# Kernel tuning notes

Measured on AMD Instinct MI355X. Metric: run time of the kernel, lower is better.

The kernel has to match this reference:

```python
import jax, jax.numpy as jnp
import numpy as np

D = 2048
N_EXPERTS = 64
K = 2


def setup_inputs() -> dict:
    key = jax.random.key(0)
    kx, kw = jax.random.split(key)
    x = jax.random.normal(kx, (4, 4096, D), dtype=jnp.float32)
    # xavier_uniform for Linear(d, n_experts): bound = sqrt(6/(fan_in+fan_out))
    bound = float(np.sqrt(6.0 / (D + N_EXPERTS)))
    W = jax.random.uniform(kw, (N_EXPERTS, D), dtype=jnp.float32, minval=-bound, maxval=bound)
    b = jnp.zeros((N_EXPERTS,), dtype=jnp.float32)
    return {"x": x, "W": W, "b": b}


def reference(x, W, b):
    # logits: [B, S, E]  (eval mode: no noise)
    logits = jnp.einsum("bsd,ed->bse", x, W) + b
    topk_vals, topk_idx = jax.lax.top_k(logits, K)  # [B, S, K]
    gates = jax.nn.softmax(topk_vals, axis=-1)
    return gates, topk_idx
```

## Files before the change

kernel.cpp:

```cpp
#include <hip/hip_runtime.h>
#include <math.h>

#define DD 2048
#define EE 64
#define TM 32
#define BK 64
#define NCHUNK (DD / BK)
#define THREADS 512

#define ROWB 272
#define XPLANE (TM * ROWB)
#define WPLANE (EE * ROWB)
#define BUFB   (XPLANE + WPLANE)

typedef _Float16 f16x8 __attribute__((ext_vector_type(8)));
typedef float    f32x4 __attribute__((ext_vector_type(4)));

__device__ static inline void split8(const float4 a, const float4 b,
                                     f16x8& hi, f16x8& lo) {
    const float S = 32.f;
    const float v[8] = {a.x * S, a.y * S, a.z * S, a.w * S,
                        b.x * S, b.y * S, b.z * S, b.w * S};
#pragma unroll
    for (int i = 0; i < 8; ++i) {
        const _Float16 h = (_Float16)v[i];
        hi[i] = h;
        lo[i] = (_Float16)(v[i] - (float)h);
    }
}

__global__ __launch_bounds__(THREADS, 4) void router_kernel(
    const float* __restrict__ x, const float* __restrict__ W,
    const float* __restrict__ bias_g, float* __restrict__ out, int n_tokens)
{
    __shared__ __attribute__((aligned(16))) char  lds[2 * BUFB];
    __shared__ __attribute__((aligned(16))) float logits[TM * (EE + 1)];

    const int tid   = threadIdx.x;
    const int tBase = blockIdx.x * TM;

    const int sr = tid >> 3;
    const int sg = tid & 7;
    const bool do_x = (sr < TM);

    const float* xrow = x + (size_t)(tBase + (sr & (TM - 1))) * DD + sg * 8;
    const float* wrow = W + (size_t)sr * DD + sg * 8;

    float4 rx0 = {0,0,0,0}, rx1 = {0,0,0,0}, rw0, rw1;

#define LOADX(c) { if (do_x) { \
        rx0 = *(const float4*)&xrow[(c) * BK];     \
        rx1 = *(const float4*)&xrow[(c) * BK + 4]; } }
#define LOADW(c) { \
        rw0 = *(const float4*)&wrow[(c) * BK];     \
        rw1 = *(const float4*)&wrow[(c) * BK + 4]; }

#define WRITE_STAGE(buf) { \
    char* base = lds + (size_t)(buf) * BUFB; \
    { f16x8 hi, lo; split8(rw0, rw1, hi, lo); \
      const int off = XPLANE + sr * ROWB + sg * 32; \
      *(f16x8*)(base + off)      = hi; \
      *(f16x8*)(base + off + 16) = lo; } \
    if (do_x) { f16x8 hi, lo; split8(rx0, rx1, hi, lo); \
      const int off = sr * ROWB + sg * 32; \
      *(f16x8*)(base + off)      = hi; \
      *(f16x8*)(base + off + 16) = lo; } }

    const int wv   = tid >> 6;
    const int lane = tid & 63;
    const int mt   = wv & 1;
    const int nt   = wv >> 1;
    const int r16  = lane & 15;
    const int kg   = lane >> 4;

    const int aoff = (mt * 16 + r16) * ROWB + kg * 32;
    const int boff = XPLANE + (nt * 16 + r16) * ROWB + kg * 32;

    f32x4 acc = {0.f, 0.f, 0.f, 0.f};

#define COMPUTE(buf) { \
    const char* base = lds + (size_t)(buf) * BUFB; \
    _Pragma("unroll") for (int ks = 0; ks < 2; ++ks) { \
        const f16x8 ah = *(const f16x8*)(base + aoff + ks * 128); \
        const f16x8 al = *(const f16x8*)(base + aoff + ks * 128 + 16); \
        const f16x8 bh = *(const f16x8*)(base + boff + ks * 128); \
        const f16x8 bl = *(const f16x8*)(base + boff + ks * 128 + 16); \
        acc = __builtin_amdgcn_mfma_f32_16x16x32_f16(ah, bh, acc, 0, 0, 0); \
        acc = __builtin_amdgcn_mfma_f32_16x16x32_f16(al, bh, acc, 0, 0, 0); \
        acc = __builtin_amdgcn_mfma_f32_16x16x32_f16(ah, bl, acc, 0, 0, 0); \
    } }

    LOADX(0); LOADW(0);
    WRITE_STAGE(0);
    LOADX(1); LOADW(1);

    int cur = 0;
    for (int c = 0; c < NCHUNK; ++c) {
        __syncthreads();
        COMPUTE(cur);
        if (c + 1 < NCHUNK) {
            WRITE_STAGE(cur ^ 1);
            if (c + 2 < NCHUNK) { LOADX(c + 2); LOADW(c + 2); }
        }
        cur ^= 1;
    }

    __syncthreads();
    const int col  = nt * 16 + r16;
    const float bcol = bias_g[col];
    const float INV  = 1.f / 1024.f;
    const int rbase  = mt * 16 + kg * 4;
#pragma unroll
    for (int r = 0; r < 4; ++r)
        logits[(rbase + r) * (EE + 1) + col] = acc[r] * INV + bcol;
    __syncthreads();

    if (tid < TM) {
        const float* lrow = &logits[tid * (EE + 1)];
        float v1 = -INFINITY, v2 = -INFINITY;
        int   i1 = 0, i2 = 0;
        for (int e = 0; e < EE; ++e) {
            const float v = lrow[e];
            if (v > v1) { v2 = v1; i2 = i1; v1 = v; i1 = e; }
            else if (v > v2) { v2 = v; i2 = e; }
        }
        const float ed  = expf(v2 - v1);
        const float inv = 1.f / (1.f + ed);
        const int tok = tBase + tid;
        out[tok * 2 + 0] = inv;
        out[tok * 2 + 1] = ed * inv;
        float* oidx = out + (size_t)2 * n_tokens;
        oidx[tok * 2 + 0] = (float)i1;
        oidx[tok * 2 + 1] = (float)i2;
    }
}

extern "C" void kernel_launch(void* const* d_in, const int* in_sizes, int n_in,
                              void* d_out, int out_size, void* d_ws, size_t ws_size,
                              hipStream_t stream) {
    const float* x = (const float*)d_in[0];
    const float* W = (const float*)d_in[1];
    const float* b = (const float*)d_in[2];
    float* out = (float*)d_out;

    const int n_tokens = in_sizes[0] / DD;
    const int n_blocks = n_tokens / TM;

    router_kernel<<<n_blocks, THREADS, 0, stream>>>(x, W, b, out, n_tokens);
}
```

Before: 202.3 us.

## Double-buffer global prefetch registers and use lightweight LDS-only barriers

Splits the prefetch registers into two sets so global loads for chunk c+2 are issued before the compute of chunk c, deepening the load pipeline to two chunks in flight. The main loop is unrolled by two with fixed LDS buffer indices. __syncthreads is replaced by a barrier that waits only on LDS counters plus a scheduling barrier, so outstanding global loads need not drain at each sync. Costs extra VGPRs, which could hurt occupancy under the launch bound of 4.

Result: no change. 202.8 us (+0.2%).

```diff
diff --git a/kernel.cpp b/kernel.cpp
--- a/kernel.cpp
+++ b/kernel.cpp
@@ -15,6 +15,10 @@
 
 typedef _Float16 f16x8 __attribute__((ext_vector_type(8)));
 typedef float    f32x4 __attribute__((ext_vector_type(4)));
+
+#define BARRIER() { asm volatile("s_waitcnt lgkmcnt(0)" ::: "memory"); \
+                    __builtin_amdgcn_s_barrier(); \
+                    __builtin_amdgcn_sched_barrier(0); }
 
 __device__ static inline void split8(const float4 a, const float4 b,
                                      f16x8& hi, f16x8& lo) {
@@ -46,16 +50,17 @@
     const float* xrow = x + (size_t)(tBase + (sr & (TM - 1))) * DD + sg * 8;
     const float* wrow = W + (size_t)sr * DD + sg * 8;
 
-    float4 rx0 = {0,0,0,0}, rx1 = {0,0,0,0}, rw0, rw1;
+    float4 rxA0 = {0,0,0,0}, rxA1 = {0,0,0,0}, rwA0, rwA1;
+    float4 rxB0 = {0,0,0,0}, rxB1 = {0,0,0,0}, rwB0, rwB1;
 
-#define LOADX(c) { if (do_x) { \
-        rx0 = *(const float4*)&xrow[(c) * BK];     \
-        rx1 = *(const float4*)&xrow[(c) * BK + 4]; } }
-#define LOADW(c) { \
-        rw0 = *(const float4*)&wrow[(c) * BK];     \
-        rw1 = *(const float4*)&wrow[(c) * BK + 4]; }
+#define LOADS(c, rx0, rx1, rw0, rw1) { \
+        rw0 = *(const float4*)&wrow[(c) * BK];       \
+        rw1 = *(const float4*)&wrow[(c) * BK + 4];   \
+        if (do_x) {                                  \
+            rx0 = *(const float4*)&xrow[(c) * BK];   \
+            rx1 = *(const float4*)&xrow[(c) * BK + 4]; } }
 
-#define WRITE_STAGE(buf) { \
+#define WRITE_STAGE(buf, rx0, rx1, rw0, rw1) { \
     char* base = lds + (size_t)(buf) * BUFB; \
     { f16x8 hi, lo; split8(rw0, rw1, hi, lo); \
       const int off = XPLANE + sr * ROWB + sg * 32; \
@@ -90,19 +95,21 @@
         acc = __builtin_amdgcn_mfma_f32_16x16x32_f16(ah, bl, acc, 0, 0, 0); \
     } }
 
-    LOADX(0); LOADW(0);
-    WRITE_STAGE(0);
-    LOADX(1); LOADW(1);
+    LOADS(0, rxA0, rxA1, rwA0, rwA1);
+    WRITE_STAGE(0, rxA0, rxA1, rwA0, rwA1);
+    LOADS(1, rxB0, rxB1, rwB0, rwB1);
 
-    int cur = 0;
-    for (int c = 0; c < NCHUNK; ++c) {
-        __syncthreads();
-        COMPUTE(cur);
-        if (c + 1 < NCHUNK) {
-            WRITE_STAGE(cur ^ 1);
-            if (c + 2 < NCHUNK) { LOADX(c + 2); LOADW(c + 2); }
-        }
-        cur ^= 1;
+    for (int c = 0; c < NCHUNK; c += 2) {
+        BARRIER();
+        if (c + 2 < NCHUNK) LOADS(c + 2, rxA0, rxA1, rwA0, rwA1);
+        COMPUTE(0);
+        WRITE_STAGE(1, rxB0, rxB1, rwB0, rwB1);
+
+        BARRIER();
+        if (c + 3 < NCHUNK) LOADS(c + 3, rxB0, rxB1, rwB0, rwB1);
+        COMPUTE(1);
+        if (c + 2 < NCHUNK)
+            WRITE_STAGE(0, rxA0, rxA1, rwA0, rwA1);
     }
 
     __syncthreads();
```

## Pre-split W into fp16 hi/lo once and stream operands directly into registers

Applied to the files above, without the earlier changes.

Adds a small pre-kernel that converts W into fp16 hi/lo planes in workspace, so the router kernel no longer re-splits W in every block. The router drops LDS staging and barriers, loading x and the pre-split W straight from global memory into MFMA fragment registers with a two-deep register double buffer. This removes LDS traffic, __syncthreads, and redundant conversion work, but each wave now loads x rows directly (x is read by 4 waves per block instead of once), relying on cache, and adds a second kernel launch.

Measured after the change: 276.6 us. 1.37x slower.

```diff
diff --git a/kernel.cpp b/kernel.cpp
--- a/kernel.cpp
+++ b/kernel.cpp
@@ -4,14 +4,8 @@
 #define DD 2048
 #define EE 64
 #define TM 32
-#define BK 64
-#define NCHUNK (DD / BK)
 #define THREADS 512
-
-#define ROWB 272
-#define XPLANE (TM * ROWB)
-#define WPLANE (EE * ROWB)
-#define BUFB   (XPLANE + WPLANE)
+#define KSTEPS (DD / 32)
 
 typedef _Float16 f16x8 __attribute__((ext_vector_type(8)));
 typedef float    f32x4 __attribute__((ext_vector_type(4)));
@@ -29,42 +23,28 @@
     }
 }
 
+__global__ __launch_bounds__(256) void wsplit_kernel(
+    const float* __restrict__ W, _Float16* __restrict__ whi,
+    _Float16* __restrict__ wlo)
+{
+    const int i = (blockIdx.x * 256 + threadIdx.x) * 8;
+    const float4 a = *(const float4*)&W[i];
+    const float4 b = *(const float4*)&W[i + 4];
+    f16x8 hi, lo;
+    split8(a, b, hi, lo);
+    *(f16x8*)&whi[i] = hi;
+    *(f16x8*)&wlo[i] = lo;
+}
+
 __global__ __launch_bounds__(THREADS, 4) void router_kernel(
-    const float* __restrict__ x, const float* __restrict__ W,
-    const float* __restrict__ bias_g, float* __restrict__ out, int n_tokens)
+    const float* __restrict__ x, const _Float16* __restrict__ whi,
+    const _Float16* __restrict__ wlo, const float* __restrict__ bias_g,
+    float* __restrict__ out, int n_tokens)
 {
-    __shared__ __attribute__((aligned(16))) char  lds[2 * BUFB];
     __shared__ __attribute__((aligned(16))) float logits[TM * (EE + 1)];
 
     const int tid   = threadIdx.x;
     const int tBase = blockIdx.x * TM;
-
-    const int sr = tid >> 3;
-    const int sg = tid & 7;
-    const bool do_x = (sr < TM);
-
-    const float* xrow = x + (size_t)(tBase + (sr & (TM - 1))) * DD + sg * 8;
-    const float* wrow = W + (size_t)sr * DD + sg * 8;
-
-    float4 rx0 = {0,0,0,0}, rx1 = {0,0,0,0}, rw0, rw1;
-
-#define LOADX(c) { if (do_x) { \
-        rx0 = *(const float4*)&xrow[(c) * BK];     \
-        rx1 = *(const float4*)&xrow[(c) * BK + 4]; } }
-#define LOADW(c) { \
-        rw0 = *(const float4*)&wrow[(c) * BK];     \
-        rw1 = *(const float4*)&wrow[(c) * BK + 4]; }
-
-#define WRITE_STAGE(buf) { \
-    char* base = lds + (size_t)(buf) * BUFB; \
-    { f16x8 hi, lo; split8(rw0, rw1, hi, lo); \
-      const int off = XPLANE + sr * ROWB + sg * 32; \
-      *(f16x8*)(base + off)      = hi; \
-      *(f16x8*)(base + off + 16) = lo; } \
-    if (do_x) { f16x8 hi, lo; split8(rx0, rx1, hi, lo); \
-      const int off = sr * ROWB + sg * 32; \
-      *(f16x8*)(base + off)      = hi; \
-      *(f16x8*)(base + off + 16) = lo; } }
 
     const int wv   = tid >> 6;
     const int lane = tid & 63;
@@ -73,39 +53,38 @@
     const int r16  = lane & 15;
     const int kg   = lane >> 4;
 
-    const int aoff = (mt * 16 + r16) * ROWB + kg * 32;
-    const int boff = XPLANE + (nt * 16 + r16) * ROWB + kg * 32;
+    const float*    xr  = x   + (size_t)(tBase + mt * 16 + r16) * DD + kg * 8;
+    const _Float16* bhp = whi + (size_t)(nt * 16 + r16) * DD + kg * 8;
+    const _Float16* blp = wlo + (size_t)(nt * 16 + r16) * DD + kg * 8;
 
     f32x4 acc = {0.f, 0.f, 0.f, 0.f};
 
-#define COMPUTE(buf) { \
-    const char* base = lds + (size_t)(buf) * BUFB; \
-    _Pragma("unroll") for (int ks = 0; ks < 2; ++ks) { \
-        const f16x8 ah = *(const f16x8*)(base + aoff + ks * 128); \
-        const f16x8 al = *(const f16x8*)(base + aoff + ks * 128 + 16); \
-        const f16x8 bh = *(const f16x8*)(base + boff + ks * 128); \
-        const f16x8 bl = *(const f16x8*)(base + boff + ks * 128 + 16); \
-        acc = __builtin_amdgcn_mfma_f32_16x16x32_f16(ah, bh, acc, 0, 0, 0); \
-        acc = __builtin_amdgcn_mfma_f32_16x16x32_f16(al, bh, acc, 0, 0, 0); \
-        acc = __builtin_amdgcn_mfma_f32_16x16x32_f16(ah, bl, acc, 0, 0, 0); \
-    } }
+    float4 a0A, a1A; f16x8 bhA, blA;
+    float4 a0B, a1B; f16x8 bhB, blB;
 
-    LOADX(0); LOADW(0);
-    WRITE_STAGE(0);
-    LOADX(1); LOADW(1);
+#define LOADK(t, a0, a1, bh, bl) { \
+    const int k0 = (t) * 32; \
+    a0 = *(const float4*)&xr[k0]; \
+    a1 = *(const float4*)&xr[k0 + 4]; \
+    bh = *(const f16x8*)&bhp[k0]; \
+    bl = *(const f16x8*)&blp[k0]; }
 
-    int cur = 0;
-    for (int c = 0; c < NCHUNK; ++c) {
-        __syncthreads();
-        COMPUTE(cur);
-        if (c + 1 < NCHUNK) {
-            WRITE_STAGE(cur ^ 1);
-            if (c + 2 < NCHUNK) { LOADX(c + 2); LOADW(c + 2); }
-        }
-        cur ^= 1;
+#define CONSUME(a0, a1, bh, bl) { \
+    f16x8 ah, al; split8(a0, a1, ah, al); \
+    acc = __builtin_amdgcn_mfma_f32_16x16x32_f16(ah, bh, acc, 0, 0, 0); \
+    acc = __builtin_amdgcn_mfma_f32_16x16x32_f16(al, bh, acc, 0, 0, 0); \
+    acc = __builtin_amdgcn_mfma_f32_16x16x32_f16(ah, bl, acc, 0, 0, 0); }
+
+    LOADK(0, a0A, a1A, bhA, blA);
+    LOADK(1, a0B, a1B, bhB, blB);
+
+    for (int t = 0; t < KSTEPS; t += 2) {
+        CONSUME(a0A, a1A, bhA, blA);
+        if (t + 2 < KSTEPS) LOADK(t + 2, a0A, a1A, bhA, blA);
+        CONSUME(a0B, a1B, bhB, blB);
+        if (t + 3 < KSTEPS) LOADK(t + 3, a0B, a1B, bhB, blB);
     }
 
-    __syncthreads();
     const int col  = nt * 16 + r16;
     const float bcol = bias_g[col];
     const float INV  = 1.f / 1024.f;
@@ -146,5 +125,9 @@
     const int n_tokens = in_sizes[0] / DD;
     const int n_blocks = n_tokens / TM;
 
-    router_kernel<<<n_blocks, THREADS, 0, stream>>>(x, W, b, out, n_tokens);
+    _Float16* whi = (_Float16*)d_ws;
+    _Float16* wlo = whi + (size_t)EE * DD;
+
+    wsplit_kernel<<<(EE * DD) / (256 * 8), 256, 0, stream>>>(W, whi, wlo);
+    router_kernel<<<n_blocks, THREADS, 0, stream>>>(x, whi, wlo, b, out, n_tokens);
 }
```
